# Optimization experiments

Hardware: AMD Instinct MI355X
Metric: run time of the kernel (lower is better)

## Reference

```python
import jax, jax.numpy as jnp
import numpy as np

B, N, T, D = 8, 32, 64, 64            # batch, nodes, time steps, node_dims
K, H, SO, HF = 4, 256, 256, 256       # edge_types, sep_hidden, sep_out, fusion hidden
E = N * (N - 1)                        # fully connected, no self loops


def setup_inputs() -> dict:
    key = jax.random.key(0)
    ks = jax.random.split(key, 12)
    inputs = jax.random.normal(ks[0], (B, N, T, D), jnp.float32)
    rel_type = jax.nn.softmax(jax.random.normal(ks[1], (B, E, K), jnp.float32), axis=-1)
    off = np.array([(i, j) for i in range(N) for j in range(N) if i != j])
    eye = np.eye(N, dtype=np.float32)
    send_mask = jnp.asarray(eye[off[:, 0]])  # [E, N] one-hot senders
    rec_mask = jnp.asarray(eye[off[:, 1]])   # [E, N] one-hot receivers
    s = 0.05
    W1 = jax.random.normal(ks[2], (K, 2 * D, H), jnp.float32) * s
    b1 = jnp.zeros((K, H), jnp.float32)
    W2 = jax.random.normal(ks[3], (K, H, SO), jnp.float32) * s
    b2 = jnp.zeros((K, SO), jnp.float32)
    Wf1 = jax.random.normal(ks[4], (D + SO, HF), jnp.float32) * s
    bf1 = jnp.zeros((HF,), jnp.float32)
    Wf2 = jax.random.normal(ks[5], (HF, HF), jnp.float32) * s
    bf2 = jnp.zeros((HF,), jnp.float32)
    Wf3 = jax.random.normal(ks[6], (HF, D), jnp.float32) * s
    bf3 = jnp.zeros((D,), jnp.float32)
    return dict(inputs=inputs, rel_type=rel_type, send_mask=send_mask, rec_mask=rec_mask,
                W1=W1, b1=b1, W2=W2, b2=b2, Wf1=Wf1, bf1=bf1, Wf2=Wf2, bf2=bf2,
                Wf3=Wf3, bf3=bf3, pred_steps=1)


def reference(inputs, rel_type, send_mask, rec_mask, W1, b1, W2, b2,
              Wf1, bf1, Wf2, bf2, Wf3, bf3, pred_steps):
    # inputs: [B, N, T, D] -> [B, T, N, D]
    x = jnp.swapaxes(inputs, 1, 2)
    t_full = x.shape[1]

    def one_step(node_input, rel):
        # NOTE: the original forward swaps send/rec masks when calling
        # one_step_ahead; reproduced faithfully here.
        send_b = jnp.einsum('en,btnd->bted', rec_mask, node_input)
        rec_b = jnp.einsum('en,btnd->bted', send_mask, node_input)
        edge_rep = jnp.concatenate([send_b, rec_b], axis=-1)  # [B,Tm,E,2D]
        fused = jnp.zeros(edge_rep.shape[:-1] + (SO,), edge_rep.dtype)
        for i in range(K):  # skip_first=False -> start at 0
            h = jax.nn.relu(edge_rep @ W1[i] + b1[i])
            h = jax.nn.relu(h @ W2[i] + b2[i])
            fused = fused + h * rel[..., i:i + 1]
        # aggregate edges -> nodes (original uses the swapped 'rec_mask',
        # which is forward's send_mask)
        agg = jnp.einsum('bted,en->btnd', fused, send_mask)
        aug = jnp.concatenate([node_input, agg], axis=-1)  # [B,Tm,N,D+SO]
        p = jax.nn.relu(aug @ Wf1 + bf1)
        p = jax.nn.relu(p @ Wf2 + bf2)
        p = p @ Wf3 + bf3
        return node_input + p

    last_pred = x[:, 0::pred_steps]                    # [B, Tm, N, D]
    curr_rel = jnp.broadcast_to(rel_type[:, None], (x.shape[0], t_full, E, K))[:, 0::pred_steps]
    preds = []
    for _ in range(pred_steps):
        last_pred = one_step(last_pred, curr_rel)
        preds.append(last_pred)
    # interleave preds back onto the original time grid
    stacked = jnp.stack(preds, axis=2)                 # [B, Tm, pred_steps, N, D]
    out = stacked.reshape(stacked.shape[0], -1, N, D)  # [B, Tm*pred_steps, N, D]
    pred_all = out[:, :t_full - 1]
    return jnp.swapaxes(pred_all, 1, 2)                # [B, N, T-1, D]
```

## Files before the change

kernel.cpp:

```cpp
#include <hip/hip_runtime.h>
#include <hip/hip_fp16.h>

typedef _Float16 f16;
typedef _Float16 f16x8 __attribute__((ext_vector_type(8)));
typedef _Float16 f16x4 __attribute__((ext_vector_type(4)));
typedef float    f32x4 __attribute__((ext_vector_type(4)));

#define AS1 __attribute__((address_space(1)))
#define AS3 __attribute__((address_space(3)))

__device__ __forceinline__ void gl_lds16(const void* g, void* l) {
    __builtin_amdgcn_global_load_lds((const AS1 unsigned int*)g,
                                     (AS3 unsigned int*)l, 16, 0, 0);
}

#define NB   8
#define NN   32
#define NT   64
#define ND   64
#define NK   4
#define NH   256
#define NSO  256
#define NE   992
#define TOUT 63
#define M1   (NB*TOUT*NN)
#define NBT  (NB*TOUT)

static constexpr size_t SZ_RS   = (size_t)M1 * 1024 * 2;
static constexpr size_t OFF_R   = 0;
static constexpr size_t OFF_S   = OFF_R + SZ_RS;
static constexpr size_t OFF_W2T = OFF_S + SZ_RS;
static constexpr size_t OFF_WF1 = OFF_W2T + 4*256*256*2;
static constexpr size_t OFF_WF2 = OFF_WF1 + 256*320*2;
static constexpr size_t OFF_WF3 = OFF_WF2 + 256*256*2;
static constexpr size_t OFF_REL = OFF_WF3 + 64*256*2;
static constexpr size_t OFF_AGG = OFF_REL + (size_t)NB*NN*NK*32*4;
static constexpr size_t OFF_W1T = OFF_AGG + (size_t)M1*256*4;

__global__ __launch_bounds__(256) void k0_prep(
    const float* __restrict__ W1, const float* __restrict__ W2,
    const float* __restrict__ Wf1, const float* __restrict__ Wf2,
    const float* __restrict__ Wf3, const float* __restrict__ rel,
    f16* __restrict__ W1T, f16* __restrict__ W2T, f16* __restrict__ Wf1T,
    f16* __restrict__ Wf2T, f16* __restrict__ Wf3T, float* __restrict__ REL,
    unsigned int* __restrict__ AGGZ)
{
    int id = blockIdx.x * 256 + threadIdx.x;
    if (id < 262144) {
        int k = id >> 16, co = (id >> 8) & 255, h = id & 255;
        W2T[id] = (f16)W2[k*65536 + h*256 + co];
    } else if (id < 344064) {
        int i = id - 262144; int co = i / 320, d = i % 320;
        Wf1T[i] = (f16)Wf1[d*256 + co];
    } else if (id < 409600) {
        int i = id - 344064; int co = i >> 8, h = i & 255;
        Wf2T[i] = (f16)Wf2[h*256 + co];
    } else if (id < 425984) {
        int i = id - 409600; int d = i >> 8, h = i & 255;
        Wf3T[i] = (f16)Wf3[h*64 + d];
    } else if (id < 458752) {
        int i = id - 425984;
        int j = i & 31, k = (i >> 5) & 3, ns = (i >> 7) & 31, b = i >> 12;
        float v = 0.f;
        if (j != ns) v = rel[(b*NE + ns*31 + (j < ns ? j : j - 1))*NK + k];
        REL[i] = v;
    } else {
        int i = id - 458752;
        int c = i >> 6, d = i & 63;
        int k = c >> 9, dd = (c >> 8) & 1, h = c & 255;
        W1T[i] = (f16)W1[(k*128 + dd*64 + d)*NH + h];
    }
    #pragma unroll
    for (int j = 0; j < 7; ++j) {
        int idx = id + j*589824;
        if (idx < 4128768) AGGZ[idx] = 0u;
    }
}

__global__ __launch_bounds__(256) void k1_partials(
    const float* __restrict__ inputs, const f16* __restrict__ W1T,
    const float* __restrict__ b1, f16* __restrict__ Rb, f16* __restrict__ Sb)
{
    __shared__ __align__(16) f16 xs[64][72];
    __shared__ __align__(16) f16 wl[256][72];
    int tid = threadIdx.x;
    int w = tid >> 6, lane = tid & 63, ln = lane & 15, q = lane >> 4;
    int m0 = blockIdx.x * 64;

    #pragma unroll
    for (int it = 0; it < 2; ++it) {
        int idx8 = it*256 + tid;
        int m = idx8 >> 3, hs = idx8 & 7;
        int mrow = m0 + m;
        int b = mrow / 2016, r2 = mrow % 2016, t = r2 >> 5, n = r2 & 31;
        const float* px = &inputs[((b*NN + n)*NT + t)*ND + hs*8];
        f32x4 v0 = *(const f32x4*)px, v1 = *(const f32x4*)(px + 4);
        f16x8 o;
        #pragma unroll
        for (int e = 0; e < 4; ++e) { o[e] = (f16)v0[e]; o[e+4] = (f16)v1[e]; }
        *(f16x8*)&xs[m][hs*8] = o;
    }
    const f32x4 z4 = {0.f, 0.f, 0.f, 0.f};
    for (int cc = 0; cc < 8; ++cc) {
        int k = cc >> 1, dd = cc & 1;
        __syncthreads();
        #pragma unroll
        for (int it = 0; it < 8; ++it) {
            int idx8 = it*256 + tid;
            int co = idx8 >> 3, seg = idx8 & 7;
            *(f16x8*)&wl[co][seg*8] = *(const f16x8*)&W1T[(size_t)(cc*256 + co)*64 + seg*8];
        }
        __syncthreads();
        f32x4 acc[16];
        #pragma unroll
        for (int nt = 0; nt < 16; ++nt) acc[nt] = z4;
        #pragma unroll
        for (int ks = 0; ks < 2; ++ks) {
            f16x8 Af = *(const f16x8*)&xs[w*16 + ln][ks*32 + q*8];
            #pragma unroll
            for (int nt = 0; nt < 16; ++nt) {
                f16x8 Bf = *(const f16x8*)&wl[nt*16 + ln][ks*32 + q*8];
                acc[nt] = __builtin_amdgcn_mfma_f32_16x16x32_f16(Af, Bf, acc[nt], 0, 0, 0);
            }
        }
        __syncthreads();
        f16* ob = &wl[0][0];
        #pragma unroll
        for (int nt = 0; nt < 16; ++nt) {
            int co = nt*16 + ln;
            float bias = dd ? b1[k*NH + co] : 0.f;
            #pragma unroll
            for (int r = 0; r < 4; ++r) {
                float v = acc[nt][r] + bias;
                ob[(w*16 + q*4 + r)*264 + co] = (f16)v;
            }
        }
        __syncthreads();
        f16* dst = dd ? Sb : Rb;
        #pragma unroll
        for (int it = 0; it < 8; ++it) {
            int idx8 = it*256 + tid;
            int m = idx8 >> 5, seg = idx8 & 31;
            int hcb = seg >> 3, c = seg & 7;
            *(f16x8*)&dst[(size_t)(m0 + m)*1024 + k*256 + hcb*64 + c*8] =
                *(const f16x8*)&ob[m*264 + hcb*64 + (((c ^ (m & 7))) << 3)];
        }
    }
}

__global__ __launch_bounds__(256, 2) void k2_edge(
    const f16* __restrict__ Rb, const f16* __restrict__ Sb,
    const f16* __restrict__ W2T, const float* __restrict__ b2,
    const float* __restrict__ REL, float* __restrict__ AGG)
{
    __shared__ __align__(16) f16 Rbuf[2][32*256];
    __shared__ __align__(16) f16 Sbuf[2][2*256];
    int tid = threadIdx.x;
    int blk = blockIdx.x;
    int k = blk & 3, g = blk >> 2;
    int ng = tid >> 6, lane = tid & 63, ln = lane & 15, q = lane >> 4;
    int lrow = lane >> 5, lseg = lane & 31;

    f16x8 Breg[4][8];
    float bias[4];
    #pragma unroll
    for (int nt = 0; nt < 4; ++nt) {
        int co = ng*64 + nt*16 + ln;
        bias[nt] = b2[k*256 + co];
        const f16* wrow = &W2T[(size_t)(k*256 + co)*256];
        #pragma unroll
        for (int ks = 0; ks < 8; ++ks)
            Breg[nt][ks] = *(const f16x8*)&wrow[ks*32 + q*8];
    }

    auto stageR = [&](int bt, int buf) {
        #pragma unroll
        for (int it = 0; it < 4; ++it) {
            int rowbase = ng*8 + it*2;
            gl_lds16(&Rb[((size_t)bt*NN + rowbase + lrow)*1024 + k*256 + lseg*8],
                     &Rbuf[buf][rowbase*256 + lane*8]);
        }
    };
    auto stageS = [&](int i, int buf) {
        int bt = g*4 + (i >> 4), nsp = i & 15;
        if (ng == 0)
            gl_lds16(&Sb[((size_t)bt*NN + nsp*2 + lrow)*1024 + k*256 + lseg*8],
                     &Sbuf[buf][lane*8]);
    };

    stageR(g*4, 0);
    stageS(0, 0);
    __syncthreads();

    const f32x4 z4 = {0.f, 0.f, 0.f, 0.f};
    const f16x8 zf = {0,0,0,0,0,0,0,0};
    for (int i = 0; i < 64; ++i) {
        int ibt = i >> 4, nsp = i & 15;
        int bt = g*4 + ibt, b = bt / TOUT;
        int rb = ibt & 1, sb = i & 1;
        if (i < 63) stageS(i + 1, sb ^ 1);
        if (nsp == 14 && ibt < 3) stageR(bt + 1, rb ^ 1);

        const f16* Rl = &Rbuf[rb][0];
        const f16* Sl = &Sbuf[sb][0];
        int ns0 = nsp*2;
        f32x4 acc[4][4];
        #pragma unroll
        for (int mt = 0; mt < 4; ++mt)
            #pragma unroll
            for (int nt = 0; nt < 4; ++nt) acc[mt][nt] = z4;

        #pragma unroll
        for (int ks = 0; ks < 8; ++ks) {
            int hc = ks >> 1;
            int c4 = (ks & 1)*4 + q;
            int paR = hc*64 + ((c4 ^ (ln & 7)) << 3);
            f16x8 rlo = *(const f16x8*)&Rl[ln*256 + paR];
            f16x8 rhi = *(const f16x8*)&Rl[(16 + ln)*256 + paR];
            f16x8 s0 = *(const f16x8*)&Sl[0*256 + hc*64 + ((c4 ^ (ns0 & 7)) << 3)];
            f16x8 s1 = *(const f16x8*)&Sl[1*256 + hc*64 + ((c4 ^ ((ns0 + 1) & 7)) << 3)];
            f16x8 A[4];
            A[0] = __builtin_elementwise_max(rlo + s0, zf);
            A[1] = __builtin_elementwise_max(rhi + s0, zf);
            A[2] = __builtin_elementwise_max(rlo + s1, zf);
            A[3] = __builtin_elementwise_max(rhi + s1, zf);
            #pragma unroll
            for (int nt = 0; nt < 4; ++nt) {
                f16x8 Bf = Breg[nt][ks];
                #pragma unroll
                for (int mt = 0; mt < 4; ++mt)
                    acc[mt][nt] = __builtin_amdgcn_mfma_f32_16x16x32_f16(
                        A[mt], Bf, acc[mt][nt], 0, 0, 0);
            }
        }
        #pragma unroll
        for (int half = 0; half < 2; ++half) {
            int ns = ns0 + half;
            const float* relp = &REL[(((size_t)b*NN + ns)*NK + k)*32];
            f32x4 rel0 = *(const f32x4*)&relp[q*4];
            f32x4 rel1 = *(const f32x4*)&relp[16 + q*4];
            #pragma unroll
            for (int nt = 0; nt < 4; ++nt) {
                float s = 0.f;
                #pragma unroll
                for (int r = 0; r < 4; ++r) {
                    float v0 = acc[2*half + 0][nt][r] + bias[nt];
                    float v1 = acc[2*half + 1][nt][r] + bias[nt];
                    v0 = v0 > 0.f ? v0 : 0.f;
                    v1 = v1 > 0.f ? v1 : 0.f;
                    s += v0 * rel0[r] + v1 * rel1[r];
                }
                s += __shfl_xor(s, 16);
                s += __shfl_xor(s, 32);
                if (lane < 16)
                    atomicAdd(&AGG[((size_t)bt*NN + ns)*256 + ng*64 + nt*16 + lane], s);
            }
        }
        __syncthreads();
    }
}

__global__ __launch_bounds__(256) void k3_node(
    const float* __restrict__ inputs, const float* __restrict__ AGG,
    const f16* __restrict__ Wf1T, const float* __restrict__ bf1,
    const f16* __restrict__ Wf2T, const float* __restrict__ bf2,
    const f16* __restrict__ Wf3T, const float* __restrict__ bf3,
    float* __restrict__ out)
{
    __shared__ __align__(16) f16 aug[64][328];
    __shared__ __align__(16) f16 p1[64][264];
    __shared__ __align__(16) f16 wl[256][72];
    int tid = threadIdx.x;
    int w = tid >> 6, lane = tid & 63, ln = lane & 15, q = lane >> 4;
    int m0 = blockIdx.x * 64;

    for (int it = 0; it < 10; ++it) {
        int s = it*256 + tid;
        if (s < 512) {
            int m = s >> 3, hs = s & 7;
            int mrow = m0 + m;
            int b = mrow / 2016, r2 = mrow % 2016, t = r2 >> 5, n = r2 & 31;
            const float* px = &inputs[((b*NN + n)*NT + t)*ND + hs*8];
            f32x4 v0 = *(const f32x4*)px, v1 = *(const f32x4*)(px + 4);
            f16x8 o;
            #pragma unroll
            for (int e = 0; e < 4; ++e) { o[e] = (f16)v0[e]; o[e+4] = (f16)v1[e]; }
            *(f16x8*)&aug[m][hs*8] = o;
        } else {
            int s2 = s - 512;
            int m = s2 >> 5, hs = s2 & 31;
            const float* pa = &AGG[(size_t)(m0 + m)*NSO + hs*8];
            f32x4 v0 = *(const f32x4*)pa, v1 = *(const f32x4*)(pa + 4);
            f16x8 o;
            #pragma unroll
            for (int e = 0; e < 4; ++e) { o[e] = (f16)v0[e]; o[e+4] = (f16)v1[e]; }
            *(f16x8*)&aug[m][64 + hs*8] = o;
        }
    }
    const f32x4 z4 = {0.f, 0.f, 0.f, 0.f};
    f32x4 acc1[16];
    #pragma unroll
    for (int nt = 0; nt < 16; ++nt) acc1[nt] = z4;
    for (int hc = 0; hc < 5; ++hc) {
        __syncthreads();
        #pragma unroll
        for (int it = 0; it < 8; ++it) {
            int idx8 = it*256 + tid;
            int co = idx8 >> 3, seg = idx8 & 7;
            *(f16x8*)&wl[co][seg*8] = *(const f16x8*)&Wf1T[co*320 + hc*64 + seg*8];
        }
        __syncthreads();
        #pragma unroll
        for (int ks = 0; ks < 2; ++ks) {
            f16x8 Af = *(const f16x8*)&aug[w*16 + ln][hc*64 + ks*32 + q*8];
            #pragma unroll
            for (int nt = 0; nt < 16; ++nt) {
                f16x8 Bf = *(const f16x8*)&wl[nt*16 + ln][ks*32 + q*8];
                acc1[nt] = __builtin_amdgcn_mfma_f32_16x16x32_f16(Af, Bf, acc1[nt], 0, 0, 0);
            }
        }
    }
    #pragma unroll
    for (int nt = 0; nt < 16; ++nt) {
        int co = nt*16 + ln;
        float bias = bf1[co];
        #pragma unroll
        for (int r = 0; r < 4; ++r) {
            float v = acc1[nt][r] + bias; v = v > 0.f ? v : 0.f;
            p1[w*16 + q*4 + r][co] = (f16)v;
        }
    }
    f32x4 acc2[16];
    #pragma unroll
    for (int nt = 0; nt < 16; ++nt) acc2[nt] = z4;
    for (int hc = 0; hc < 4; ++hc) {
        __syncthreads();
        #pragma unroll
        for (int it = 0; it < 8; ++it) {
            int idx8 = it*256 + tid;
            int co = idx8 >> 3, seg = idx8 & 7;
            *(f16x8*)&wl[co][seg*8] = *(const f16x8*)&Wf2T[co*256 + hc*64 + seg*8];
        }
        __syncthreads();
        #pragma unroll
        for (int ks = 0; ks < 2; ++ks) {
            f16x8 Af = *(const f16x8*)&p1[w*16 + ln][hc*64 + ks*32 + q*8];
            #pragma unroll
            for (int nt = 0; nt < 16; ++nt) {
                f16x8 Bf = *(const f16x8*)&wl[nt*16 + ln][ks*32 + q*8];
                acc2[nt] = __builtin_amdgcn_mfma_f32_16x16x32_f16(Af, Bf, acc2[nt], 0, 0, 0);
            }
        }
    }
    f16* p2 = &aug[0][0];
    #pragma unroll
    for (int nt = 0; nt < 16; ++nt) {
        int co = nt*16 + ln;
        float bias = bf2[co];
        #pragma unroll
        for (int r = 0; r < 4; ++r) {
            float v = acc2[nt][r] + bias; v = v > 0.f ? v : 0.f;
            p2[(w*16 + q*4 + r)*264 + co] = (f16)v;
        }
    }
    __syncthreads();
    f16* w3 = &wl[0][0];
    #pragma unroll
    for (int it = 0; it < 8; ++it) {
        int idx8 = it*256 + tid;
        int d = idx8 >> 5, seg = idx8 & 31;
        *(f16x8*)&w3[d*264 + seg*8] = *(const f16x8*)&Wf3T[d*256 + seg*8];
    }
    __syncthreads();
    f32x4 acc3[4];
    #pragma unroll
    for (int nt = 0; nt < 4; ++nt) acc3[nt] = z4;
    #pragma unroll
    for (int ks = 0; ks < 8; ++ks) {
        f16x8 Af = *(const f16x8*)&p2[(w*16 + ln)*264 + ks*32 + q*8];
        #pragma unroll
        for (int nt = 0; nt < 4; ++nt) {
            f16x8 Bf = *(const f16x8*)&w3[(nt*16 + ln)*264 + ks*32 + q*8];
            acc3[nt] = __builtin_amdgcn_mfma_f32_16x16x32_f16(Af, Bf, acc3[nt], 0, 0, 0);
        }
    }
    #pragma unroll
    for (int nt = 0; nt < 4; ++nt) {
        int d = nt*16 + ln;
        float bias = bf3[d];
        #pragma unroll
        for (int r = 0; r < 4; ++r) {
            int mrow = m0 + w*16 + q*4 + r;
            int b = mrow / 2016, r2 = mrow % 2016, t = r2 >> 5, n = r2 & 31;
            float xv = inputs[((b*NN + n)*NT + t)*ND + d];
            out[((size_t)(b*NN + n)*TOUT + t)*ND + d] = acc3[nt][r] + bias + xv;
        }
    }
}

extern "C" void kernel_launch(void* const* d_in, const int* in_sizes, int n_in,
                              void* d_out, int out_size, void* d_ws, size_t ws_size,
                              hipStream_t stream)
{
    const float* inputs = (const float*)d_in[0];
    const float* rel    = (const float*)d_in[1];
    const float* W1     = (const float*)d_in[4];
    const float* b1     = (const float*)d_in[5];
    const float* W2     = (const float*)d_in[6];
    const float* b2     = (const float*)d_in[7];
    const float* Wf1    = (const float*)d_in[8];
    const float* bf1    = (const float*)d_in[9];
    const float* Wf2    = (const float*)d_in[10];
    const float* bf2    = (const float*)d_in[11];
    const float* Wf3    = (const float*)d_in[12];
    const float* bf3    = (const float*)d_in[13];
    char* ws = (char*)d_ws;
    f16*   Rb   = (f16*)(ws + OFF_R);
    f16*   Sb   = (f16*)(ws + OFF_S);
    f16*   W2T  = (f16*)(ws + OFF_W2T);
    f16*   Wf1T = (f16*)(ws + OFF_WF1);
    f16*   Wf2T = (f16*)(ws + OFF_WF2);
    f16*   Wf3T = (f16*)(ws + OFF_WF3);
    float* REL  = (float*)(ws + OFF_REL);
    float* AGG  = (float*)(ws + OFF_AGG);
    f16*   W1T  = (f16*)(ws + OFF_W1T);
    float* out  = (float*)d_out;

    hipLaunchKernelGGL(k0_prep, dim3(2304), dim3(256), 0, stream,
                       W1, W2, Wf1, Wf2, Wf3, rel, W1T, W2T, Wf1T, Wf2T, Wf3T, REL,
                       (unsigned int*)AGG);
    hipLaunchKernelGGL(k1_partials, dim3(252), dim3(256), 0, stream,
                       inputs, W1T, b1, Rb, Sb);
    hipLaunchKernelGGL(k2_edge, dim3(504), dim3(256), 0, stream,
                       Rb, Sb, W2T, b2, REL, AGG);
    hipLaunchKernelGGL(k3_node, dim3(252), dim3(256), 0, stream,
                       inputs, AGG, Wf1T, bf1, Wf2T, bf2, Wf3T, bf3, out);
}
```

Baseline: 464.2 us.

## Stage all sender rows per timestep and sync once per bt instead of per pair

The edge kernel now loads the full 32-row sender tile alongside the receiver tile for each (batch,time) step into double-buffered LDS. The inner loop over 16 sender pairs runs without any barrier, so there is one __syncthreads per time step rather than one per sender pair (64 down to 4). Per-iteration small S loads by a single wave are removed. The cost is about 32 KB more LDS per block, which could lower occupancy under the 2-blocks-per-CU launch bound.

```diff
diff --git a/kernel.cpp b/kernel.cpp
--- a/kernel.cpp
+++ b/kernel.cpp
@@ -154,7 +154,7 @@
     const float* __restrict__ REL, float* __restrict__ AGG)
 {
     __shared__ __align__(16) f16 Rbuf[2][32*256];
-    __shared__ __align__(16) f16 Sbuf[2][2*256];
+    __shared__ __align__(16) f16 Sbuf[2][32*256];
     int tid = threadIdx.x;
     int blk = blockIdx.x;
     int k = blk & 3, g = blk >> 2;
@@ -173,87 +173,81 @@
             Breg[nt][ks] = *(const f16x8*)&wrow[ks*32 + q*8];
     }
 
-    auto stageR = [&](int bt, int buf) {
+    auto stageRS = [&](int bt, int buf) {
         #pragma unroll
         for (int it = 0; it < 4; ++it) {
             int rowbase = ng*8 + it*2;
-            gl_lds16(&Rb[((size_t)bt*NN + rowbase + lrow)*1024 + k*256 + lseg*8],
-                     &Rbuf[buf][rowbase*256 + lane*8]);
+            size_t goff = ((size_t)bt*NN + rowbase + lrow)*1024 + k*256 + lseg*8;
+            gl_lds16(&Rb[goff], &Rbuf[buf][rowbase*256 + lane*8]);
+            gl_lds16(&Sb[goff], &Sbuf[buf][rowbase*256 + lane*8]);
         }
     };
-    auto stageS = [&](int i, int buf) {
-        int bt = g*4 + (i >> 4), nsp = i & 15;
-        if (ng == 0)
-            gl_lds16(&Sb[((size_t)bt*NN + nsp*2 + lrow)*1024 + k*256 + lseg*8],
-                     &Sbuf[buf][lane*8]);
-    };
-
-    stageR(g*4, 0);
-    stageS(0, 0);
+
+    stageRS(g*4, 0);
     __syncthreads();
 
     const f32x4 z4 = {0.f, 0.f, 0.f, 0.f};
     const f16x8 zf = {0,0,0,0,0,0,0,0};
-    for (int i = 0; i < 64; ++i) {
-        int ibt = i >> 4, nsp = i & 15;
+    for (int ibt = 0; ibt < 4; ++ibt) {
         int bt = g*4 + ibt, b = bt / TOUT;
-        int rb = ibt & 1, sb = i & 1;
-        if (i < 63) stageS(i + 1, sb ^ 1);
-        if (nsp == 14 && ibt < 3) stageR(bt + 1, rb ^ 1);
-
-        const f16* Rl = &Rbuf[rb][0];
-        const f16* Sl = &Sbuf[sb][0];
-        int ns0 = nsp*2;
-        f32x4 acc[4][4];
-        #pragma unroll
-        for (int mt = 0; mt < 4; ++mt)
-            #pragma unroll
-            for (int nt = 0; nt < 4; ++nt) acc[mt][nt] = z4;
-
-        #pragma unroll
-        for (int ks = 0; ks < 8; ++ks) {
-            int hc = ks >> 1;
-            int c4 = (ks & 1)*4 + q;
-            int paR = hc*64 + ((c4 ^ (ln & 7)) << 3);
-            f16x8 rlo = *(const f16x8*)&Rl[ln*256 + paR];
-            f16x8 rhi = *(const f16x8*)&Rl[(16 + ln)*256 + paR];
-            f16x8 s0 = *(const f16x8*)&Sl[0*256 + hc*64 + ((c4 ^ (ns0 & 7)) << 3)];
-            f16x8 s1 = *(const f16x8*)&Sl[1*256 + hc*64 + ((c4 ^ ((ns0 + 1) & 7)) << 3)];
-            f16x8 A[4];
-            A[0] = __builtin_elementwise_max(rlo + s0, zf);
-            A[1] = __builtin_elementwise_max(rhi + s0, zf);
-            A[2] = __builtin_elementwise_max(rlo + s1, zf);
-            A[3] = __builtin_elementwise_max(rhi + s1, zf);
-            #pragma unroll
-            for (int nt = 0; nt < 4; ++nt) {
-                f16x8 Bf = Breg[nt][ks];
+        int buf = ibt & 1;
+        if (ibt < 3) stageRS(bt + 1, buf ^ 1);
+        const f16* Rl = &Rbuf[buf][0];
+        const f16* Sl = &Sbuf[buf][0];
+
+        for (int nsp = 0; nsp < 16; ++nsp) {
+            int ns0 = nsp*2;
+            f32x4 acc[4][4];
+            #pragma unroll
+            for (int mt = 0; mt < 4; ++mt)
                 #pragma unroll
-                for (int mt = 0; mt < 4; ++mt)
-                    acc[mt][nt] = __builtin_amdgcn_mfma_f32_16x16x32_f16(
-                        A[mt], Bf, acc[mt][nt], 0, 0, 0);
-            }
-        }
-        #pragma unroll
-        for (int half = 0; half < 2; ++half) {
-            int ns = ns0 + half;
-            const float* relp = &REL[(((size_t)b*NN + ns)*NK + k)*32];
-            f32x4 rel0 = *(const f32x4*)&relp[q*4];
-            f32x4 rel1 = *(const f32x4*)&relp[16 + q*4];
-            #pragma unroll
-            for (int nt = 0; nt < 4; ++nt) {
-                float s = 0.f;
+                for (int nt = 0; nt < 4; ++nt) acc[mt][nt] = z4;
+
+            #pragma unroll
+            for (int ks = 0; ks < 8; ++ks) {
+                int hc = ks >> 1;
+                int c4 = (ks & 1)*4 + q;
+                int paR = hc*64 + ((c4 ^ (ln & 7)) << 3);
+                f16x8 rlo = *(const f16x8*)&Rl[ln*256 + paR];
+                f16x8 rhi = *(const f16x8*)&Rl[(16 + ln)*256 + paR];
+                f16x8 s0 = *(const f16x8*)&Sl[(ns0 + 0)*256 + hc*64 + ((c4 ^ (ns0 & 7)) << 3)];
+                f16x8 s1 = *(const f16x8*)&Sl[(ns0 + 1)*256 + hc*64 + ((c4 ^ ((ns0 + 1) & 7)) << 3)];
+                f16x8 A[4];
+                A[0] = __builtin_elementwise_max(rlo + s0, zf);
+                A[1] = __builtin_elementwise_max(rhi + s0, zf);
+                A[2] = __builtin_elementwise_max(rlo + s1, zf);
+                A[3] = __builtin_elementwise_max(rhi + s1, zf);
                 #pragma unroll
-                for (int r = 0; r < 4; ++r) {
-                    float v0 = acc[2*half + 0][nt][r] + bias[nt];
-                    float v1 = acc[2*half + 1][nt][r] + bias[nt];
-                    v0 = v0 > 0.f ? v0 : 0.f;
-                    v1 = v1 > 0.f ? v1 : 0.f;
-                    s += v0 * rel0[r] + v1 * rel1[r];
+                for (int nt = 0; nt < 4; ++nt) {
+                    f16x8 Bf = Breg[nt][ks];
+                    #pragma unroll
+                    for (int mt = 0; mt < 4; ++mt)
+                        acc[mt][nt] = __builtin_amdgcn_mfma_f32_16x16x32_f16(
+                            A[mt], Bf, acc[mt][nt], 0, 0, 0);
                 }
-                s += __shfl_xor(s, 16);
-                s += __shfl_xor(s, 32);
-                if (lane < 16)
-                    atomicAdd(&AGG[((size_t)bt*NN + ns)*256 + ng*64 + nt*16 + lane], s);
+            }
+            #pragma unroll
+            for (int half = 0; half < 2; ++half) {
+                int ns = ns0 + half;
+                const float* relp = &REL[(((size_t)b*NN + ns)*NK + k)*32];
+                f32x4 rel0 = *(const f32x4*)&relp[q*4];
+                f32x4 rel1 = *(const f32x4*)&relp[16 + q*4];
+                #pragma unroll
+                for (int nt = 0; nt < 4; ++nt) {
+                    float s = 0.f;
+                    #pragma unroll
+                    for (int r = 0; r < 4; ++r) {
+                        float v0 = acc[2*half + 0][nt][r] + bias[nt];
+                        float v1 = acc[2*half + 1][nt][r] + bias[nt];
+                        v0 = v0 > 0.f ? v0 : 0.f;
+                        v1 = v1 > 0.f ? v1 : 0.f;
+                        s += v0 * rel0[r] + v1 * rel1[r];
+                    }
+                    s += __shfl_xor(s, 16);
+                    s += __shfl_xor(s, 32);
+                    if (lane < 16)
+                        atomicAdd(&AGG[((size_t)bt*NN + ns)*256 + ng*64 + nt*16 + lane], s);
+                }
             }
         }
         __syncthreads();
```

New measurement: 559.1 us. 20.4% more time.

## Quad-buffer sender tiles, halve edge-loop barriers, fold bias into accumulator init

Applied to the files above, without the earlier changes.

The S staging buffer in the edge kernel grows from two slots to four and is prefetched two iterations ahead. This allows a block barrier only on every other iteration. The S rows are now stored unswizzled (the producer skips the XOR swizzle when dd is set), which makes the S loads simpler. The second-layer bias is used as the MFMA accumulator's initial value, removing per-element adds. Risks are LDS bank conflicts on the unswizzled S reads and correctness of the R-buffer reuse now that barriers are skipped.

```diff
diff --git a/kernel.cpp b/kernel.cpp
--- a/kernel.cpp
+++ b/kernel.cpp
@@ -142,8 +142,9 @@
             int idx8 = it*256 + tid;
             int m = idx8 >> 5, seg = idx8 & 31;
             int hcb = seg >> 3, c = seg & 7;
+            int cs = dd ? c : (c ^ (m & 7));
             *(f16x8*)&dst[(size_t)(m0 + m)*1024 + k*256 + hcb*64 + c*8] =
-                *(const f16x8*)&ob[m*264 + hcb*64 + (((c ^ (m & 7))) << 3)];
+                *(const f16x8*)&ob[m*264 + hcb*64 + (cs << 3)];
         }
     }
 }
@@ -154,7 +155,7 @@
     const float* __restrict__ REL, float* __restrict__ AGG)
 {
     __shared__ __align__(16) f16 Rbuf[2][32*256];
-    __shared__ __align__(16) f16 Sbuf[2][2*256];
+    __shared__ __align__(16) f16 Sbuf[4][2*256];
     int tid = threadIdx.x;
     int blk = blockIdx.x;
     int k = blk & 3, g = blk >> 2;
@@ -162,11 +163,13 @@
     int lrow = lane >> 5, lseg = lane & 31;
 
     f16x8 Breg[4][8];
-    float bias[4];
+    f32x4 bini[4];
     #pragma unroll
     for (int nt = 0; nt < 4; ++nt) {
         int co = ng*64 + nt*16 + ln;
-        bias[nt] = b2[k*256 + co];
+        float bv = b2[k*256 + co];
+        f32x4 bb = {bv, bv, bv, bv};
+        bini[nt] = bb;
         const f16* wrow = &W2T[(size_t)(k*256 + co)*256];
         #pragma unroll
         for (int ks = 0; ks < 8; ++ks)
@@ -181,44 +184,45 @@
                      &Rbuf[buf][rowbase*256 + lane*8]);
         }
     };
-    auto stageS = [&](int i, int buf) {
+    auto stageS = [&](int i, int slot) {
         int bt = g*4 + (i >> 4), nsp = i & 15;
         if (ng == 0)
             gl_lds16(&Sb[((size_t)bt*NN + nsp*2 + lrow)*1024 + k*256 + lseg*8],
-                     &Sbuf[buf][lane*8]);
+                     &Sbuf[slot][lane*8]);
     };
 
     stageR(g*4, 0);
     stageS(0, 0);
+    stageS(1, 1);
     __syncthreads();
 
-    const f32x4 z4 = {0.f, 0.f, 0.f, 0.f};
     const f16x8 zf = {0,0,0,0,0,0,0,0};
     for (int i = 0; i < 64; ++i) {
         int ibt = i >> 4, nsp = i & 15;
         int bt = g*4 + ibt, b = bt / TOUT;
-        int rb = ibt & 1, sb = i & 1;
-        if (i < 63) stageS(i + 1, sb ^ 1);
+        int rb = ibt & 1;
+        if (i < 62) stageS(i + 2, (i + 2) & 3);
         if (nsp == 14 && ibt < 3) stageR(bt + 1, rb ^ 1);
 
         const f16* Rl = &Rbuf[rb][0];
-        const f16* Sl = &Sbuf[sb][0];
+        const f16* Sl = &Sbuf[i & 3][0];
         int ns0 = nsp*2;
         f32x4 acc[4][4];
         #pragma unroll
         for (int mt = 0; mt < 4; ++mt)
             #pragma unroll
-            for (int nt = 0; nt < 4; ++nt) acc[mt][nt] = z4;
+            for (int nt = 0; nt < 4; ++nt) acc[mt][nt] = bini[nt];
 
         #pragma unroll
         for (int ks = 0; ks < 8; ++ks) {
             int hc = ks >> 1;
             int c4 = (ks & 1)*4 + q;
             int paR = hc*64 + ((c4 ^ (ln & 7)) << 3);
+            int paS = hc*64 + c4*8;
             f16x8 rlo = *(const f16x8*)&Rl[ln*256 + paR];
             f16x8 rhi = *(const f16x8*)&Rl[(16 + ln)*256 + paR];
-            f16x8 s0 = *(const f16x8*)&Sl[0*256 + hc*64 + ((c4 ^ (ns0 & 7)) << 3)];
-            f16x8 s1 = *(const f16x8*)&Sl[1*256 + hc*64 + ((c4 ^ ((ns0 + 1) & 7)) << 3)];
+            f16x8 s0 = *(const f16x8*)&Sl[0*256 + paS];
+            f16x8 s1 = *(const f16x8*)&Sl[1*256 + paS];
             f16x8 A[4];
             A[0] = __builtin_elementwise_max(rlo + s0, zf);
             A[1] = __builtin_elementwise_max(rhi + s0, zf);
@@ -244,8 +248,8 @@
                 float s = 0.f;
                 #pragma unroll
                 for (int r = 0; r < 4; ++r) {
-                    float v0 = acc[2*half + 0][nt][r] + bias[nt];
-                    float v1 = acc[2*half + 1][nt][r] + bias[nt];
+                    float v0 = acc[2*half + 0][nt][r];
+                    float v1 = acc[2*half + 1][nt][r];
                     v0 = v0 > 0.f ? v0 : 0.f;
                     v1 = v1 > 0.f ? v1 : 0.f;
                     s += v0 * rel0[r] + v1 * rel1[r];
@@ -256,7 +260,7 @@
                     atomicAdd(&AGG[((size_t)bt*NN + ns)*256 + ng*64 + nt*16 + lane], s);
             }
         }
-        __syncthreads();
+        if (i & 1) __syncthreads();
     }
 }
 
```

New measurement: 475.9 us. 2.5% more time.
